# Optimization experiments

Hardware: AMD Instinct MI355X
Metric: run time of the kernel (lower is better)

Reference implementation:

```python
import jax, jax.numpy as jnp
import numpy as np

N_NODES = 100000
N_EDGES = 3200000
B = 64            # number of graphs / RNA batch
DIM = 16          # GINE hidden dim
NFP = 33          # protein node feature dim
EMB = 128         # embedding dim
MAXLEN = 3000     # rna_global length (conv1d in_channels)
LOCLEN = 2998     # rna_local length = 3000 - log4(64) + 1
NF = 32           # n_filters
KS = 8            # conv kernel size -> 128-8+1 = 121
FC_IN = NF * 121  # 3872
BN_EPS = 1e-5


def setup_inputs() -> dict:
    key = jax.random.key(0)
    ks = jax.random.split(key, 32)
    s = 0.1
    p = {}
    # forward data args
    p['pro_x'] = jax.random.normal(ks[0], (N_NODES, NFP), jnp.float32)
    p['pro_edge_index'] = jax.random.randint(ks[1], (2, N_EDGES), 0, N_NODES, jnp.int32)
    p['pro_weight'] = jax.random.uniform(ks[2], (N_EDGES, 1), jnp.float32)
    p['pro_batch'] = jnp.sort(jax.random.randint(ks[3], (N_NODES,), 0, B, jnp.int32))
    p['rna_global'] = jax.random.randint(ks[4], (B, MAXLEN), 0, 5, jnp.int32)
    p['rna_local'] = jax.random.randint(ks[5], (B, LOCLEN), 0, 65, jnp.int32)
    # GINE layer 1 (33 -> 16)
    p['g1_w1'] = jax.random.normal(ks[6], (NFP, DIM), jnp.float32) * s
    p['g1_b1'] = jnp.zeros((DIM,), jnp.float32)
    p['g1_w2'] = jax.random.normal(ks[7], (DIM, DIM), jnp.float32) * s
    p['g1_b2'] = jnp.zeros((DIM,), jnp.float32)
    p['g1_ew'] = jax.random.normal(ks[8], (1, NFP), jnp.float32) * s  # edge Linear(1, 33)
    p['g1_eb'] = jnp.zeros((NFP,), jnp.float32)
    p['g1_eps'] = jnp.zeros((), jnp.float32)
    # GINE layers 2-5 (16 -> 16), stacked on leading axis
    p['g_w1'] = jax.random.normal(ks[9], (4, DIM, DIM), jnp.float32) * s
    p['g_b1'] = jnp.zeros((4, DIM), jnp.float32)
    p['g_w2'] = jax.random.normal(ks[10], (4, DIM, DIM), jnp.float32) * s
    p['g_b2'] = jnp.zeros((4, DIM), jnp.float32)
    p['g_ew'] = jax.random.normal(ks[11], (4, 1, DIM), jnp.float32) * s  # edge Linear(1, 16)
    p['g_eb'] = jnp.zeros((4, DIM), jnp.float32)
    p['g_eps'] = jnp.zeros((4,), jnp.float32)
    # BatchNorm1d x5
    p['bn_gamma'] = jnp.ones((5, DIM), jnp.float32)
    p['bn_beta'] = jnp.zeros((5, DIM), jnp.float32)
    # fc1_xp (16 -> 128)
    p['fc1_xp_w'] = jax.random.normal(ks[12], (DIM, EMB), jnp.float32) * s
    p['fc1_xp_b'] = jnp.zeros((EMB,), jnp.float32)
    # RNA branch
    p['emb1'] = jax.random.normal(ks[13], (5, EMB), jnp.float32)
    p['emb2'] = jax.random.normal(ks[14], (65, EMB), jnp.float32)
    p['convr1_w'] = jax.random.normal(ks[15], (NF, MAXLEN, KS), jnp.float32) * 0.01
    p['convr1_b'] = jnp.zeros((NF,), jnp.float32)
    p['convr2_w'] = jax.random.normal(ks[16], (NF, LOCLEN, KS), jnp.float32) * 0.01
    p['convr2_b'] = jnp.zeros((NF,), jnp.float32)
    p['fcxr_w'] = jax.random.normal(ks[17], (FC_IN, EMB), jnp.float32) * 0.01
    p['fcxr_b'] = jnp.zeros((EMB,), jnp.float32)
    return p


def _gine(x, src, dst, ew, w1, b1, w2, b2, ew_w, ew_b, eps):
    # GINEConv: out = MLP((1+eps)*x + sum_j relu(x_j + edge_lin(e_ij)))
    e = ew @ ew_w + ew_b                       # [E, d]
    m = jax.nn.relu(x[src] + e)                # [E, d] gather + fuse
    agg = jax.ops.segment_sum(m, dst, num_segments=N_NODES)
    h = (1.0 + eps) * x + agg
    return jax.nn.relu(h @ w1 + b1) @ w2 + b2


def _bn(x, gamma, beta):
    mu = jnp.mean(x, axis=0)
    var = jnp.var(x, axis=0)
    return (x - mu) * jax.lax.rsqrt(var + BN_EPS) * gamma + beta


def _rna_branch(tokens, emb, cw, cb, fcw, fcb):
    x = emb[tokens]                            # [B, L, 128]
    y = jax.lax.conv_general_dilated(x, cw, (1,), 'VALID',
                                     dimension_numbers=('NCH', 'OIH', 'NCH'))
    y = y + cb[None, :, None]                  # [B, 32, 121]
    return y.reshape(y.shape[0], -1) @ fcw + fcb


def reference(pro_x, pro_edge_index, pro_weight, pro_batch, rna_global, rna_local,
              g1_w1, g1_b1, g1_w2, g1_b2, g1_ew, g1_eb, g1_eps,
              g_w1, g_b1, g_w2, g_b2, g_ew, g_eb, g_eps,
              bn_gamma, bn_beta, fc1_xp_w, fc1_xp_b,
              emb1, emb2, convr1_w, convr1_b, convr2_w, convr2_b, fcxr_w, fcxr_b):
    src, dst = pro_edge_index[0], pro_edge_index[1]
    # RNA global / local branches (shared fc_xr)
    xrg = _rna_branch(rna_global, emb1, convr1_w, convr1_b, fcxr_w, fcxr_b)
    xrl = _rna_branch(rna_local, emb2, convr2_w, convr2_b, fcxr_w, fcxr_b)
    # protein GINE stack
    xp = jax.nn.relu(_gine(pro_x, src, dst, pro_weight,
                           g1_w1, g1_b1, g1_w2, g1_b2, g1_ew, g1_eb, g1_eps))
    xp = _bn(xp, bn_gamma[0], bn_beta[0])
    for i in range(4):
        xp = jax.nn.relu(_gine(xp, src, dst, pro_weight,
                               g_w1[i], g_b1[i], g_w2[i], g_b2[i],
                               g_ew[i], g_eb[i], g_eps[i]))
        xp = _bn(xp, bn_gamma[i + 1], bn_beta[i + 1])
    # global mean pool over graphs
    sums = jax.ops.segment_sum(xp, pro_batch, num_segments=B)
    cnt = jax.ops.segment_sum(jnp.ones((N_NODES, 1), xp.dtype), pro_batch, num_segments=B)
    xp = jax.nn.relu((sums / jnp.maximum(cnt, 1.0)) @ fc1_xp_w + fc1_xp_b)
    # dropout in eval mode -> identity
    xc_rna = 0.5 * (xrg + xrl)
    return (xc_rna, xp)
```

## Files before the change

### kernel.cpp

```cpp
#include <hip/hip_runtime.h>
#include <hip/hip_fp16.h>

#define N_NODES 100000
#define N_EDGES 3200000
#define BGR 64
#define DIM 16
#define NFP 33
#define ROW1 32
#define H1STR 36
#define EMB 128
#define MAXLEN 3000
#define LOCLEN 2998
#define NF 32
#define KS 8
#define OUTT 121
#define FC_IN 3872
#define BN_EPSV 1e-5f
#define POOL_CHUNK 256
#define POOL_BLKS 391
#define MLPB 391
#define AGGB1 6250
#define AGGB16 3125
#define NBIN 391
#define BCNT_BLK 512
#define P1_CHUNK 4096
#define P1_BLOCKS 782
#define MAXBIN 9088
#define NKC 32
#define KCH 121
#define WDEC (1.f / 32767.f)

__global__ void __launch_bounds__(256) k_bincnt(const int* __restrict__ dst,
                                                int* __restrict__ bh) {
    __shared__ int hist[NBIN];
    int t = threadIdx.x, bid = blockIdx.x;
    for (int b = t; b < NBIN; b += 256) hist[b] = 0;
    __syncthreads();
    int e0 = bid * (N_EDGES / BCNT_BLK);
    int e1 = e0 + (N_EDGES / BCNT_BLK);
    for (int e = e0 + t; e < e1; e += 256) atomicAdd(&hist[dst[e] >> 8], 1);
    __syncthreads();
    for (int b = t; b < NBIN; b += 256) bh[b * BCNT_BLK + bid] = hist[b];
}

__global__ void __launch_bounds__(512) k_binscan(const int* __restrict__ bh,
                                                 int* __restrict__ binoff,
                                                 int* __restrict__ bincur) {
    __shared__ int sc[512];
    int t = threadIdx.x;
    int s = 0;
    if (t < NBIN) {
        const int4* row = (const int4*)(bh + t * BCNT_BLK);
        #pragma unroll 4
        for (int k = 0; k < BCNT_BLK / 4; k++) {
            int4 v = row[k];
            s += v.x + v.y + v.z + v.w;
        }
    }
    sc[t] = s;
    __syncthreads();
    for (int off = 1; off < 512; off <<= 1) {
        int v = (t >= off) ? sc[t - off] : 0;
        __syncthreads();
        sc[t] += v;
        __syncthreads();
    }
    int excl = sc[t] - s;
    if (t <= NBIN) binoff[t] = excl;
    if (t < NBIN) bincur[t] = excl;
}

__global__ void __launch_bounds__(256) k_part1(const int* __restrict__ src,
                                               const int* __restrict__ dst,
                                               const float* __restrict__ w,
                                               int* __restrict__ bincur,
                                               int2* __restrict__ tmp_sw) {
    __shared__ int2 srec[P1_CHUNK];
    __shared__ unsigned short sbin[P1_CHUNK];
    __shared__ unsigned short sperm[P1_CHUNK];
    __shared__ int hist[NBIN];
    __shared__ int off[NBIN];
    __shared__ int cur[NBIN];
    __shared__ int base[NBIN];
    __shared__ int sc[512];
    int t = threadIdx.x;
    int g0 = blockIdx.x * P1_CHUNK;
    int cn = N_EDGES - g0; if (cn > P1_CHUNK) cn = P1_CHUNK;
    for (int b = t; b < NBIN; b += 256) hist[b] = 0;
    __syncthreads();
    for (int j = t; j < cn; j += 256) {
        int d = dst[g0 + j];
        int b = d >> 8;
        sbin[j] = (unsigned short)b;
        srec[j] = make_int2(src[g0 + j] | ((d & 255) << 20), __float_as_int(w[g0 + j]));
        atomicAdd(&hist[b], 1);
    }
    __syncthreads();
    sc[t] = (t < NBIN) ? hist[t] : 0;
    sc[256 + t] = (256 + t < NBIN) ? hist[256 + t] : 0;
    __syncthreads();
    for (int o = 1; o <= 256; o <<= 1) {
        int v0 = (t >= o) ? sc[t - o] : 0;
        int v1 = sc[256 + t - o];
        __syncthreads();
        sc[t] += v0;
        sc[256 + t] += v1;
        __syncthreads();
    }
    for (int b = t; b < NBIN; b += 256) {
        int e = sc[b] - hist[b];
        off[b] = e;
        cur[b] = e;
        int c = hist[b];
        base[b] = c ? atomicAdd(&bincur[b], c) : 0;
    }
    __syncthreads();
    for (int j = t; j < cn; j += 256) {
        int p = atomicAdd(&cur[sbin[j]], 1);
        sperm[p] = (unsigned short)j;
    }
    __syncthreads();
    for (int p = t; p < cn; p += 256) {
        int j = sperm[p];
        int b = sbin[j];
        tmp_sw[base[b] + (p - off[b])] = srec[j];
    }
}

__global__ void __launch_bounds__(256) k_part2(const int2* __restrict__ tmp_sw,
                                               const int* __restrict__ binoff,
                                               unsigned* __restrict__ er,
                                               int* __restrict__ ptr) {
    __shared__ unsigned char sdl[MAXBIN];
    __shared__ unsigned short perm[MAXBIN];
    __shared__ int hist[256];
    __shared__ int cur[256];
    __shared__ int sc[256];
    int t = threadIdx.x, b = blockIdx.x;
    int nlo = b << 8;
    int e0 = binoff[b], e1 = binoff[b + 1];
    int cnt = e1 - e0;
    int stage = cnt < MAXBIN ? cnt : MAXBIN;
    hist[t] = 0;
    __syncthreads();
    for (int j = t; j < stage; j += 256) {
        unsigned char dl = (unsigned char)((tmp_sw[e0 + j].x >> 20) & 255);
        sdl[j] = dl;
        atomicAdd(&hist[dl], 1);
    }
    for (int j = stage + t; j < cnt; j += 256)
        atomicAdd(&hist[(tmp_sw[e0 + j].x >> 20) & 255], 1);
    __syncthreads();
    int v = hist[t];
    sc[t] = v;
    __syncthreads();
    for (int off = 1; off < 256; off <<= 1) {
        int u = (t >= off) ? sc[t - off] : 0;
        __syncthreads();
        sc[t] += u;
        __syncthreads();
    }
    int excl = sc[t] - v;
    cur[t] = excl;
    if (nlo + t < N_NODES) ptr[nlo + t] = e0 + excl;
    if (b == NBIN - 1 && t == 0) ptr[N_NODES] = N_EDGES;
    __syncthreads();
    for (int j = t; j < stage; j += 256) {
        int p = atomicAdd(&cur[sdl[j]], 1);
        perm[p] = (unsigned short)j;
    }
    __syncthreads();
    for (int j = stage + t; j < cnt; j += 256) {
        int2 sw = tmp_sw[e0 + j];
        int p = atomicAdd(&cur[(sw.x >> 20) & 255], 1);
        unsigned wq = (unsigned)(__int_as_float(sw.y) * 32767.f + 0.5f);
        er[e0 + p] = ((unsigned)sw.x & 0x1FFFFu) | (wq << 17);
    }
    for (int p = t; p < stage; p += 256) {
        int2 sw = tmp_sw[e0 + perm[p]];
        unsigned wq = (unsigned)(__int_as_float(sw.y) * 32767.f + 0.5f);
        er[e0 + p] = ((unsigned)sw.x & 0x1FFFFu) | (wq << 17);
    }
}

__global__ void k_half1(const float* __restrict__ x, __half* __restrict__ xh,
                        __half* __restrict__ xh32) {
    int i = blockIdx.x * blockDim.x + threadIdx.x;
    if (i < N_NODES * NFP) {
        int n = i / NFP, f = i - n * NFP;
        __half v = __float2half(x[i]);
        if (f < 32) xh[n * ROW1 + f] = v;
        else xh32[n] = v;
    }
}

__global__ void __launch_bounds__(256) k_cwt(const float* __restrict__ cw,
                                             float* __restrict__ cwT, int L) {
    int l = blockIdx.x;
    int ok = threadIdx.x;
    cwT[l * 256 + ok] = cw[(ok >> 3) * (L * KS) + l * KS + (ok & 7)];
}

__device__ __forceinline__ void acc8p(float a[8], uint4 r, float wv,
                                      const float* __restrict__ ewf,
                                      const float* __restrict__ ebf) {
    float2 f01 = __half22float2(*(__half2*)&r.x);
    float2 f23 = __half22float2(*(__half2*)&r.y);
    float2 f45 = __half22float2(*(__half2*)&r.z);
    float2 f67 = __half22float2(*(__half2*)&r.w);
    float x[8] = {f01.x, f01.y, f23.x, f23.y, f45.x, f45.y, f67.x, f67.y};
    #pragma unroll
    for (int j = 0; j < 8; j++)
        a[j] += fmaxf(x[j] + fmaf(wv, ewf[j], ebf[j]), 0.f);
}

__device__ __forceinline__ void acc8s(float a[8], uint4 r, float wv,
                                      const float* __restrict__ scf,
                                      const float* __restrict__ cbf,
                                      const float* __restrict__ ewf) {
    float2 f01 = __half22float2(*(__half2*)&r.x);
    float2 f23 = __half22float2(*(__half2*)&r.y);
    float2 f45 = __half22float2(*(__half2*)&r.z);
    float2 f67 = __half22float2(*(__half2*)&r.w);
    float x[8] = {f01.x, f01.y, f23.x, f23.y, f45.x, f45.y, f67.x, f67.y};
    #pragma unroll
    for (int j = 0; j < 8; j++)
        a[j] += fmaxf(fmaf(x[j], scf[j], fmaf(wv, ewf[j], cbf[j])), 0.f);
}

__global__ void __launch_bounds__(256) k_agg1(
    const __half* __restrict__ xh, const __half* __restrict__ xh32,
    const int* __restrict__ ptr, const unsigned* __restrict__ er,
    const float* __restrict__ ew, const float* __restrict__ ebv,
    const float* __restrict__ epsp, float* __restrict__ h) {
    int t = threadIdx.x;
    int wave = t >> 6, lane = t & 63;
    int nl = lane >> 4;
    int slot = (lane >> 2) & 3;
    int q = lane & 3;
    float ewf[8], ebf[8];
    #pragma unroll
    for (int j = 0; j < 8; j++) { ewf[j] = ew[q * 8 + j]; ebf[j] = ebv[q * 8 + j]; }
    float ew32 = ew[32], eb32 = ebv[32];
    float ep = 1.f + epsp[0];
    int node = blockIdx.x * 16 + wave * 4 + nl;
    int e0 = ptr[node], e1 = ptr[node + 1];
    float a[8] = {0, 0, 0, 0, 0, 0, 0, 0};
    float a32 = 0.f;
    int i = e0 + slot;
    while (i + 12 < e1) {
        unsigned ev0 = er[i], ev1 = er[i + 4], ev2 = er[i + 8], ev3 = er[i + 12];
        int s0 = ev0 & 0x1FFFF, s1 = ev1 & 0x1FFFF;
        int s2 = ev2 & 0x1FFFF, s3 = ev3 & 0x1FFFF;
        float wv0 = (float)(ev0 >> 17) * WDEC;
        float wv1 = (float)(ev1 >> 17) * WDEC;
        float wv2 = (float)(ev2 >> 17) * WDEC;
        float wv3 = (float)(ev3 >> 17) * WDEC;
        uint4 r0 = *(const uint4*)(xh + s0 * ROW1 + q * 8);
        uint4 r1 = *(const uint4*)(xh + s1 * ROW1 + q * 8);
        uint4 r2 = *(const uint4*)(xh + s2 * ROW1 + q * 8);
        uint4 r3 = *(const uint4*)(xh + s3 * ROW1 + q * 8);
        acc8p(a, r0, wv0, ewf, ebf);
        acc8p(a, r1, wv1, ewf, ebf);
        acc8p(a, r2, wv2, ewf, ebf);
        acc8p(a, r3, wv3, ewf, ebf);
        if (q == 0) {
            a32 += fmaxf(__half2float(xh32[s0]) + fmaf(wv0, ew32, eb32), 0.f);
            a32 += fmaxf(__half2float(xh32[s1]) + fmaf(wv1, ew32, eb32), 0.f);
            a32 += fmaxf(__half2float(xh32[s2]) + fmaf(wv2, ew32, eb32), 0.f);
            a32 += fmaxf(__half2float(xh32[s3]) + fmaf(wv3, ew32, eb32), 0.f);
        }
        i += 16;
    }
    while (i < e1) {
        unsigned ev = er[i];
        int s = ev & 0x1FFFF;
        float wv = (float)(ev >> 17) * WDEC;
        uint4 r = *(const uint4*)(xh + s * ROW1 + q * 8);
        acc8p(a, r, wv, ewf, ebf);
        if (q == 0)
            a32 += fmaxf(__half2float(xh32[s]) + fmaf(wv, ew32, eb32), 0.f);
        i += 4;
    }
    #pragma unroll
    for (int j = 0; j < 8; j++) {
        a[j] += __shfl_xor(a[j], 4);
        a[j] += __shfl_xor(a[j], 8);
    }
    a32 += __shfl_xor(a32, 4);
    a32 += __shfl_xor(a32, 8);
    if (slot == 0) {
        uint4 sraw = *(const uint4*)(xh + node * ROW1 + q * 8);
        float2 s01 = __half22float2(*(__half2*)&sraw.x);
        float2 s23 = __half22float2(*(__half2*)&sraw.y);
        float2 s45 = __half22float2(*(__half2*)&sraw.z);
        float2 s67 = __half22float2(*(__half2*)&sraw.w);
        float* hp = h + node * H1STR + q * 8;
        *(float4*)hp = make_float4(ep * s01.x + a[0], ep * s01.y + a[1],
                                   ep * s23.x + a[2], ep * s23.y + a[3]);
        *(float4*)(hp + 4) = make_float4(ep * s45.x + a[4], ep * s45.y + a[5],
                                         ep * s67.x + a[6], ep * s67.y + a[7]);
        if (q == 0)
            h[node * H1STR + 32] = ep * __half2float(xh32[node]) + a32;
    }
}

__global__ void __launch_bounds__(256) k_agg16(
    const __half* __restrict__ zh, const int* __restrict__ ptr,
    const unsigned* __restrict__ er,
    const float* __restrict__ ew, const float* __restrict__ ebv,
    const float* __restrict__ epsp,
    const float* __restrict__ bnstat, const float* __restrict__ gamma,
    const float* __restrict__ beta, float* __restrict__ h) {
    int t = threadIdx.x;
    int wave = t >> 6, lane = t & 63;
    int nl = lane >> 3;
    int slot = (lane >> 1) & 3;
    int hh = lane & 1;
    float ep = 1.f + epsp[0];
    const float invn = 1.f / (float)N_NODES;
    float scf[8], shf[8], cbf[8], ewf[8];
    #pragma unroll
    for (int j = 0; j < 8; j++) {
        int f = hh * 8 + j;
        float mu = bnstat[f] * invn;
        float var = bnstat[DIM + f] * invn - mu * mu;
        float sc = gamma[f] * rsqrtf(var + BN_EPSV);
        scf[j] = sc;
        shf[j] = beta[f] - mu * sc;
        cbf[j] = shf[j] + ebv[f];
        ewf[j] = ew[f];
    }
    int node = blockIdx.x * 32 + wave * 8 + nl;
    int e0 = ptr[node], e1 = ptr[node + 1];
    float a[8] = {0, 0, 0, 0, 0, 0, 0, 0};
    int i = e0 + slot;
    while (i + 12 < e1) {
        unsigned ev0 = er[i], ev1 = er[i + 4], ev2 = er[i + 8], ev3 = er[i + 12];
        float wv0 = (float)(ev0 >> 17) * WDEC;
        float wv1 = (float)(ev1 >> 17) * WDEC;
        float wv2 = (float)(ev2 >> 17) * WDEC;
        float wv3 = (float)(ev3 >> 17) * WDEC;
        uint4 r0 = *(const uint4*)(zh + (ev0 & 0x1FFFFu) * DIM + hh * 8);
        uint4 r1 = *(const uint4*)(zh + (ev1 & 0x1FFFFu) * DIM + hh * 8);
        uint4 r2 = *(const uint4*)(zh + (ev2 & 0x1FFFFu) * DIM + hh * 8);
        uint4 r3 = *(const uint4*)(zh + (ev3 & 0x1FFFFu) * DIM + hh * 8);
        acc8s(a, r0, wv0, scf, cbf, ewf);
        acc8s(a, r1, wv1, scf, cbf, ewf);
        acc8s(a, r2, wv2, scf, cbf, ewf);
        acc8s(a, r3, wv3, scf, cbf, ewf);
        i += 16;
    }
    while (i < e1) {
        unsigned ev = er[i];
        float wv = (float)(ev >> 17) * WDEC;
        uint4 r = *(const uint4*)(zh + (ev & 0x1FFFFu) * DIM + hh * 8);
        acc8s(a, r, wv, scf, cbf, ewf);
        i += 4;
    }
    #pragma unroll
    for (int j = 0; j < 8; j++) a[j] += __shfl_xor(a[j], 2);
    #pragma unroll
    for (int j = 0; j < 8; j++) a[j] += __shfl_xor(a[j], 4);
    if (slot == 0) {
        uint4 sraw = *(const uint4*)(zh + node * DIM + hh * 8);
        float2 s01 = __half22float2(*(__half2*)&sraw.x);
        float2 s23 = __half22float2(*(__half2*)&sraw.y);
        float2 s45 = __half22float2(*(__half2*)&sraw.z);
        float2 s67 = __half22float2(*(__half2*)&sraw.w);
        float xs[8] = {s01.x, s01.y, s23.x, s23.y, s45.x, s45.y, s67.x, s67.y};
        float o8[8];
        #pragma unroll
        for (int j = 0; j < 8; j++)
            o8[j] = ep * fmaf(xs[j], scf[j], shf[j]) + a[j];
        float* hp = h + node * DIM + hh * 8;
        *(float4*)hp = make_float4(o8[0], o8[1], o8[2], o8[3]);
        *(float4*)(hp + 4) = make_float4(o8[4], o8[5], o8[6], o8[7]);
    }
}

__device__ __forceinline__ void mlp_bn_tail(float zv[16], bool active, int t,
                                            float* __restrict__ part) {
    __shared__ float red[4][32];
    float zs[16], zq[16];
    #pragma unroll
    for (int o = 0; o < 16; o++) {
        zs[o] = active ? zv[o] : 0.f;
        zq[o] = active ? zv[o] * zv[o] : 0.f;
    }
    #pragma unroll
    for (int m = 1; m <= 32; m <<= 1) {
        #pragma unroll
        for (int o = 0; o < 16; o++) {
            zs[o] += __shfl_xor(zs[o], m);
            zq[o] += __shfl_xor(zq[o], m);
        }
    }
    int wave = t >> 6, lane = t & 63;
    if (lane == 0) {
        #pragma unroll
        for (int o = 0; o < 16; o++) {
            red[wave][o] = zs[o];
            red[wave][16 + o] = zq[o];
        }
    }
    __syncthreads();
    if (t < 32)
        part[blockIdx.x * 32 + t] = red[0][t] + red[1][t] + red[2][t] + red[3][t];
}

__device__ __forceinline__ void store_zh(__half* __restrict__ zh, int n, float zv[16]) {
    __half2 p[8];
    #pragma unroll
    for (int j = 0; j < 8; j++) p[j] = __floats2half2_rn(zv[2 * j], zv[2 * j + 1]);
    *(uint4*)(zh + n * DIM) = *(uint4*)&p[0];
    *(uint4*)(zh + n * DIM + 8) = *(uint4*)&p[4];
}

__global__ void __launch_bounds__(256) k_mlp16(
    const float* __restrict__ h,
    const float* __restrict__ W1, const float* __restrict__ b1,
    const float* __restrict__ W2, const float* __restrict__ b2,
    __half* __restrict__ zh, float* __restrict__ part) {
    __shared__ float W1s[256], W2s[256], b1s[16], b2s[16];
    int t = threadIdx.x;
    W1s[t] = W1[t];
    W2s[t] = W2[t];
    if (t < 16) { b1s[t] = b1[t]; b2s[t] = b2[t]; }
    __syncthreads();
    int n = blockIdx.x * 256 + t;
    bool active = n < N_NODES;
    float zv[16];
    if (active) {
        float hv[16];
        #pragma unroll
        for (int j = 0; j < 4; j++) {
            float4 v = *(const float4*)(h + n * DIM + j * 4);
            hv[j * 4] = v.x; hv[j * 4 + 1] = v.y; hv[j * 4 + 2] = v.z; hv[j * 4 + 3] = v.w;
        }
        float tv[16];
        #pragma unroll
        for (int o = 0; o < 16; o++) {
            float s = b1s[o];
            #pragma unroll
            for (int f = 0; f < 16; f++) s += hv[f] * W1s[f * 16 + o];
            tv[o] = fmaxf(s, 0.f);
        }
        #pragma unroll
        for (int o = 0; o < 16; o++) {
            float s = b2s[o];
            #pragma unroll
            for (int f = 0; f < 16; f++) s += tv[f] * W2s[f * 16 + o];
            zv[o] = fmaxf(s, 0.f);
        }
        store_zh(zh, n, zv);
    }
    mlp_bn_tail(zv, active, t, part);
}

__global__ void __launch_bounds__(256) k_mlp1(
    const float* __restrict__ h,
    const float* __restrict__ W1, const float* __restrict__ b1,
    const float* __restrict__ W2, const float* __restrict__ b2,
    __half* __restrict__ zh, float* __restrict__ part) {
    __shared__ float W1s[NFP * 16], W2s[256], b1s[16], b2s[16];
    int t = threadIdx.x;
    for (int j = t; j < NFP * 16; j += 256) W1s[j] = W1[j];
    W2s[t] = W2[t];
    if (t < 16) { b1s[t] = b1[t]; b2s[t] = b2[t]; }
    __syncthreads();
    int n = blockIdx.x * 256 + t;
    bool active = n < N_NODES;
    float zv[16];
    if (active) {
        float hv[NFP];
        #pragma unroll
        for (int j = 0; j < 8; j++) {
            float4 v = *(const float4*)(h + n * H1STR + j * 4);
            hv[j * 4] = v.x; hv[j * 4 + 1] = v.y; hv[j * 4 + 2] = v.z; hv[j * 4 + 3] = v.w;
        }
        hv[32] = h[n * H1STR + 32];
        float tv[16];
        #pragma unroll
        for (int o = 0; o < 16; o++) {
            float s = b1s[o];
            #pragma unroll
            for (int f = 0; f < NFP; f++) s += hv[f] * W1s[f * 16 + o];
            tv[o] = fmaxf(s, 0.f);
        }
        #pragma unroll
        for (int o = 0; o < 16; o++) {
            float s = b2s[o];
            #pragma unroll
            for (int f = 0; f < 16; f++) s += tv[f] * W2s[f * 16 + o];
            zv[o] = fmaxf(s, 0.f);
        }
        store_zh(zh, n, zv);
    }
    mlp_bn_tail(zv, active, t, part);
}

__global__ void __launch_bounds__(1024) k_bnred(const float* __restrict__ part,
                                                float* __restrict__ bnstat) {
    __shared__ float red[1024];
    int t = threadIdx.x;
    int f = t & 31, g = t >> 5;
    float s = 0.f;
    for (int i = g; i < MLPB; i += 32) s += part[i * 32 + f];
    red[t] = s;
    __syncthreads();
    for (int off = 512; off >= 32; off >>= 1) {
        if (t < off) red[t] += red[t + off];
        __syncthreads();
    }
    if (t < 32) bnstat[t] = red[t];
}

__global__ void __launch_bounds__(256) k_pool(const __half* __restrict__ zh,
                                              const int* __restrict__ batch,
                                              const float* __restrict__ bnstat,
                                              const float* __restrict__ gamma,
                                              const float* __restrict__ beta,
                                              float* __restrict__ gsum,
                                              float* __restrict__ gcnt) {
    __shared__ float lsum[BGR * DIM];
    __shared__ float lcnt[BGR];
    int t = threadIdx.x;
    for (int j = t; j < BGR * DIM; j += 256) lsum[j] = 0.f;
    if (t < BGR) lcnt[t] = 0.f;
    __syncthreads();
    int f = t & 15, r = t >> 4;
    const float invn = 1.f / (float)N_NODES;
    float mu = bnstat[f] * invn;
    float var = bnstat[DIM + f] * invn - mu * mu;
    float sc = gamma[f] * rsqrtf(var + BN_EPSV);
    float sh = beta[f] - mu * sc;
    int start = blockIdx.x * POOL_CHUNK;
    float acc = 0.f, cacc = 0.f;
    int cur = -1;
    for (int i = 0; i < POOL_CHUNK / 16; i++) {
        int n = start + r + i * 16;
        if (n >= N_NODES) break;
        int b = batch[n];
        if (b != cur) {
            if (cur >= 0) {
                atomicAdd(&lsum[cur * DIM + f], acc);
                if (f == 0) atomicAdd(&lcnt[cur], cacc);
            }
            cur = b; acc = 0.f; cacc = 0.f;
        }
        acc += fmaf(__half2float(zh[n * DIM + f]), sc, sh);
        cacc += 1.f;
    }
    if (cur >= 0) {
        atomicAdd(&lsum[cur * DIM + f], acc);
        if (f == 0) atomicAdd(&lcnt[cur], cacc);
    }
    __syncthreads();
    for (int j = t; j < BGR * DIM; j += 256) {
        float v = lsum[j];
        if (v != 0.f) atomicAdd(&gsum[j], v);
    }
    if (t < BGR) {
        float v = lcnt[t];
        if (v != 0.f) atomicAdd(&gcnt[t], v);
    }
}

__global__ void k_xp(const float* __restrict__ gsum, const float* __restrict__ gcnt,
                     const float* __restrict__ w, const float* __restrict__ bias,
                     float* __restrict__ out) {
    int b = blockIdx.x;
    int e = threadIdx.x;
    float inv = 1.f / fmaxf(gcnt[b], 1.f);
    float acc = bias[e];
    #pragma unroll
    for (int f = 0; f < DIM; f++) acc += gsum[b * DIM + f] * inv * w[f * EMB + e];
    out[b * EMB + e] = fmaxf(acc, 0.f);
}

__global__ void __launch_bounds__(256) k_bucket(const int* __restrict__ tok, int L, int V,
                                                int* __restrict__ blist,
                                                int* __restrict__ bptr) {
    __shared__ int hist[65];
    __shared__ int cursor[65];
    int b = blockIdx.x, t = threadIdx.x;
    if (t < V) hist[t] = 0;
    __syncthreads();
    for (int l = t; l < L; l += 256) atomicAdd(&hist[tok[b * L + l]], 1);
    __syncthreads();
    if (t == 0) {
        int run = 0;
        for (int v = 0; v < V; v++) {
            cursor[v] = run;
            bptr[b * (V + 1) + v] = run;
            run += hist[v];
        }
        bptr[b * (V + 1) + V] = run;
    }
    __syncthreads();
    for (int l = t; l < L; l += 256) {
        int v = tok[b * L + l];
        int p = atomicAdd(&cursor[v], 1);
        blist[b * L + p] = l;
    }
}

__global__ void __launch_bounds__(256) k_wsum(const int* __restrict__ blist,
                                              const int* __restrict__ bptr,
                                              const float* __restrict__ cwT,
                                              float* __restrict__ W, int L, int V) {
    int b = blockIdx.x, v = blockIdx.y;
    int t = threadIdx.x;
    int s = bptr[b * (V + 1) + v], e = bptr[b * (V + 1) + v + 1];
    const int* bl = blist + b * L;
    float acc = 0.f;
    int j = s;
    while (j + 3 < e) {
        int t0 = bl[j], t1 = bl[j + 1], t2 = bl[j + 2], t3 = bl[j + 3];
        float a0 = cwT[t0 * 256 + t];
        float a1 = cwT[t1 * 256 + t];
        float a2 = cwT[t2 * 256 + t];
        float a3 = cwT[t3 * 256 + t];
        acc += a0 + a1 + a2 + a3;
        j += 4;
    }
    while (j < e) {
        acc += cwT[bl[j] * 256 + t];
        j++;
    }
    int o = t >> 3, k = t & 7;
    W[((b * NF + o) * V + v) * KS + k] = acc;
}

__global__ void k_y(const float* __restrict__ Wg, const float* __restrict__ Wl,
                    const float* __restrict__ emb1, const float* __restrict__ emb2,
                    const float* __restrict__ cb1, const float* __restrict__ cb2,
                    float* __restrict__ yg, float* __restrict__ yl) {
    int which = blockIdx.y;
    int bo = blockIdx.x;
    int b = bo >> 5, o = bo & 31;
    int t = threadIdx.x;
    const float* W = which ? Wl : Wg;
    const float* emb = which ? emb2 : emb1;
    const float* cb = which ? cb2 : cb1;
    float* y = which ? yl : yg;
    int V = which ? 65 : 5;
    __shared__ float Wsh[65 * KS];
    const float* Wrow = W + (b * NF + o) * V * KS;
    for (int j = t; j < V * KS; j += 128) Wsh[j] = Wrow[j];
    __syncthreads();
    if (t < OUTT) {
        float acc = cb[o];
        for (int v = 0; v < V; v++) {
            const float* ep = emb + v * EMB + t;
            #pragma unroll
            for (int k = 0; k < KS; k++) acc += Wsh[v * KS + k] * ep[k];
        }
        y[(b * NF + o) * OUTT + t] = acc;
    }
}

__global__ void __launch_bounds__(128) k_fcpart(const float* __restrict__ yg,
                                                const float* __restrict__ yl,
                                                const float* __restrict__ w,
                                                float* __restrict__ partial) {
    int b = blockIdx.x, which = blockIdx.y, kc = blockIdx.z;
    const float* y = which ? yl : yg;
    int e = threadIdx.x;
    __shared__ float ych[KCH];
    int j0 = kc * KCH;
    if (e < KCH) ych[e] = y[b * FC_IN + j0 + e];
    __syncthreads();
    float acc = 0.f;
    #pragma unroll 4
    for (int jj = 0; jj < KCH; jj++) acc += ych[jj] * w[(j0 + jj) * EMB + e];
    partial[((which * BGR + b) * NKC + kc) * EMB + e] = acc;
}

__global__ void k_fcred(const float* __restrict__ partial, const float* __restrict__ bias,
                        float* __restrict__ out) {
    int b = blockIdx.x;
    int e = threadIdx.x;
    const float* pg = partial + b * NKC * EMB + e;
    const float* pl = partial + (BGR + b) * NKC * EMB + e;
    float ag = bias[e], al = bias[e];
    #pragma unroll
    for (int k = 0; k < NKC; k++) { ag += pg[k * EMB]; al += pl[k * EMB]; }
    out[b * EMB + e] = 0.5f * (ag + al);
}

extern "C" void kernel_launch(void* const* d_in, const int* in_sizes, int n_in,
                              void* d_out, int out_size, void* d_ws, size_t ws_size,
                              hipStream_t stream) {
    const float* pro_x = (const float*)d_in[0];
    const int* eidx = (const int*)d_in[1];
    const int* esrc = eidx;
    const int* edst = eidx + N_EDGES;
    const float* pw = (const float*)d_in[2];
    const int* batch = (const int*)d_in[3];
    const int* rg = (const int*)d_in[4];
    const int* rl = (const int*)d_in[5];
    const float* g1_w1 = (const float*)d_in[6];
    const float* g1_b1 = (const float*)d_in[7];
    const float* g1_w2 = (const float*)d_in[8];
    const float* g1_b2 = (const float*)d_in[9];
    const float* g1_ew = (const float*)d_in[10];
    const float* g1_eb = (const float*)d_in[11];
    const float* g1_eps = (const float*)d_in[12];
    const float* g_w1 = (const float*)d_in[13];
    const float* g_b1 = (const float*)d_in[14];
    const float* g_w2 = (const float*)d_in[15];
    const float* g_b2 = (const float*)d_in[16];
    const float* g_ew = (const float*)d_in[17];
    const float* g_eb = (const float*)d_in[18];
    const float* g_eps = (const float*)d_in[19];
    const float* bn_gamma = (const float*)d_in[20];
    const float* bn_beta = (const float*)d_in[21];
    const float* fc1_xp_w = (const float*)d_in[22];
    const float* fc1_xp_b = (const float*)d_in[23];
    const float* emb1 = (const float*)d_in[24];
    const float* emb2 = (const float*)d_in[25];
    const float* convr1_w = (const float*)d_in[26];
    const float* convr1_b = (const float*)d_in[27];
    const float* convr2_w = (const float*)d_in[28];
    const float* convr2_b = (const float*)d_in[29];
    const float* fcxr_w = (const float*)d_in[30];
    const float* fcxr_b = (const float*)d_in[31];
    float* out = (float*)d_out;

    float* wsf = (float*)d_ws;
    int* ptr       = (int*)wsf;        wsf += 100128;
    int* binoff    = (int*)wsf;        wsf += 512;
    int* bincur    = (int*)wsf;        wsf += 512;
    unsigned* er   = (unsigned*)wsf;   wsf += 2 * N_EDGES;
    float* stats   = wsf;              wsf += 1280;
    float* un = wsf;
    int2* tmp_sw          = (int2*)un;
    int* bh               = (int*)(un + 7200000);
    float* cwTg  = un;
    float* cwTl  = un + 768000;
    __half* zh   = (__half*)(un + 1600000);
    __half* xh1  = (__half*)(un + 2400000);
    __half* xh32 = (__half*)(un + 4000000);
    float* bpart = un + 4100000;
    float* Wg    = un + 4300000;
    float* Wl    = un + 4382000;
    float* yg    = un + 5447000;
    float* yl    = un + 5695000;
    int* blg     = (int*)(un + 5961000);
    int* bll     = (int*)(un + 6153000);
    int* bpg     = (int*)(un + 6345000);
    int* bpl     = (int*)(un + 6346000);
    float* fcpart = un + 6360000;
    float* h      = un + 7400000;
    float* gsum   = stats;
    float* gcnt   = stats + 1024;
    float* bnstat = stats + 1088;

    hipMemsetAsync(stats, 0, 1280 * sizeof(float), stream);

    k_bincnt<<<BCNT_BLK, 256, 0, stream>>>(edst, bh);
    k_binscan<<<1, 512, 0, stream>>>(bh, binoff, bincur);
    k_part1<<<P1_BLOCKS, 256, 0, stream>>>(esrc, edst, pw, bincur, tmp_sw);
    k_part2<<<NBIN, 256, 0, stream>>>(tmp_sw, binoff, er, ptr);

    k_cwt<<<MAXLEN, 256, 0, stream>>>(convr1_w, cwTg, MAXLEN);
    k_cwt<<<LOCLEN, 256, 0, stream>>>(convr2_w, cwTl, LOCLEN);

    k_half1<<<(N_NODES * NFP + 255) / 256, 256, 0, stream>>>(pro_x, xh1, xh32);

    k_bucket<<<BGR, 256, 0, stream>>>(rg, MAXLEN, 5, blg, bpg);
    k_bucket<<<BGR, 256, 0, stream>>>(rl, LOCLEN, 65, bll, bpl);
    k_wsum<<<dim3(BGR, 5), 256, 0, stream>>>(blg, bpg, cwTg, Wg, MAXLEN, 5);
    k_wsum<<<dim3(BGR, 65), 256, 0, stream>>>(bll, bpl, cwTl, Wl, LOCLEN, 65);
    k_y<<<dim3(BGR * NF, 2), 128, 0, stream>>>(Wg, Wl, emb1, emb2, convr1_b, convr2_b, yg, yl);
    k_fcpart<<<dim3(BGR, 2, NKC), 128, 0, stream>>>(yg, yl, fcxr_w, fcpart);
    k_fcred<<<BGR, 128, 0, stream>>>(fcpart, fcxr_b, out);

    k_agg1<<<AGGB1, 256, 0, stream>>>(xh1, xh32, ptr, er, g1_ew, g1_eb, g1_eps, h);
    k_mlp1<<<MLPB, 256, 0, stream>>>(h, g1_w1, g1_b1, g1_w2, g1_b2, zh, bpart);
    k_bnred<<<1, 1024, 0, stream>>>(bpart, bnstat);
    for (int i = 0; i < 4; i++) {
        k_agg16<<<AGGB16, 256, 0, stream>>>(zh, ptr, er,
                                            g_ew + i * DIM, g_eb + i * DIM, g_eps + i,
                                            bnstat + i * 32, bn_gamma + i * DIM,
                                            bn_beta + i * DIM, h);
        k_mlp16<<<MLPB, 256, 0, stream>>>(h, g_w1 + i * DIM * DIM, g_b1 + i * DIM,
                                          g_w2 + i * DIM * DIM, g_b2 + i * DIM, zh, bpart);
        k_bnred<<<1, 1024, 0, stream>>>(bpart, bnstat + (i + 1) * 32);
    }
    k_pool<<<POOL_BLKS, 256, 0, stream>>>(zh, batch, bnstat + 4 * 32,
                                          bn_gamma + 4 * DIM, bn_beta + 4 * DIM, gsum, gcnt);
    k_xp<<<BGR, EMB, 0, stream>>>(gsum, gcnt, fc1_xp_w, fc1_xp_b, out + BGR * EMB);
}
```

Measured before the change: 649.2 us.

## Split global RNA weight-sum into segments and reduce edge-loop unroll to two

The global-RNA k_wsum launch only had 320 blocks, each walking about 600 positions serially. It is now split eight ways per (batch, token), writing partial sums that k_y reduces when it loads its weights. This raises parallelism on the long serial chains. Separately, both GINE aggregation kernels cut their edge-gather unroll from four to two loads per iteration, which lowers register pressure but leaves fewer loads in flight. The workspace layout is reshuffled to fit the larger partial buffer.

```diff
diff --git a/kernel.cpp b/kernel.cpp
--- a/kernel.cpp
+++ b/kernel.cpp
@@ -29,6 +29,7 @@
 #define NKC 32
 #define KCH 121
 #define WDEC (1.f / 32767.f)
+#define SEG_G 8
 
 __global__ void __launch_bounds__(256) k_bincnt(const int* __restrict__ dst,
                                                 int* __restrict__ bh) {
@@ -248,31 +249,23 @@
     float a[8] = {0, 0, 0, 0, 0, 0, 0, 0};
     float a32 = 0.f;
     int i = e0 + slot;
-    while (i + 12 < e1) {
-        unsigned ev0 = er[i], ev1 = er[i + 4], ev2 = er[i + 8], ev3 = er[i + 12];
+    while (i + 4 < e1) {
+        unsigned ev0 = er[i];
+        unsigned ev1 = er[i + 4];
         int s0 = ev0 & 0x1FFFF, s1 = ev1 & 0x1FFFF;
-        int s2 = ev2 & 0x1FFFF, s3 = ev3 & 0x1FFFF;
         float wv0 = (float)(ev0 >> 17) * WDEC;
         float wv1 = (float)(ev1 >> 17) * WDEC;
-        float wv2 = (float)(ev2 >> 17) * WDEC;
-        float wv3 = (float)(ev3 >> 17) * WDEC;
         uint4 r0 = *(const uint4*)(xh + s0 * ROW1 + q * 8);
         uint4 r1 = *(const uint4*)(xh + s1 * ROW1 + q * 8);
-        uint4 r2 = *(const uint4*)(xh + s2 * ROW1 + q * 8);
-        uint4 r3 = *(const uint4*)(xh + s3 * ROW1 + q * 8);
         acc8p(a, r0, wv0, ewf, ebf);
         acc8p(a, r1, wv1, ewf, ebf);
-        acc8p(a, r2, wv2, ewf, ebf);
-        acc8p(a, r3, wv3, ewf, ebf);
         if (q == 0) {
             a32 += fmaxf(__half2float(xh32[s0]) + fmaf(wv0, ew32, eb32), 0.f);
             a32 += fmaxf(__half2float(xh32[s1]) + fmaf(wv1, ew32, eb32), 0.f);
-            a32 += fmaxf(__half2float(xh32[s2]) + fmaf(wv2, ew32, eb32), 0.f);
-            a32 += fmaxf(__half2float(xh32[s3]) + fmaf(wv3, ew32, eb32), 0.f);
-        }
-        i += 16;
-    }
-    while (i < e1) {
+        }
+        i += 8;
+    }
+    if (i < e1) {
         unsigned ev = er[i];
         int s = ev & 0x1FFFF;
         float wv = (float)(ev >> 17) * WDEC;
@@ -280,7 +273,6 @@
         acc8p(a, r, wv, ewf, ebf);
         if (q == 0)
             a32 += fmaxf(__half2float(xh32[s]) + fmaf(wv, ew32, eb32), 0.f);
-        i += 4;
     }
     #pragma unroll
     for (int j = 0; j < 8; j++) {
@@ -335,28 +327,22 @@
     int e0 = ptr[node], e1 = ptr[node + 1];
     float a[8] = {0, 0, 0, 0, 0, 0, 0, 0};
     int i = e0 + slot;
-    while (i + 12 < e1) {
-        unsigned ev0 = er[i], ev1 = er[i + 4], ev2 = er[i + 8], ev3 = er[i + 12];
+    while (i + 4 < e1) {
+        unsigned ev0 = er[i];
+        unsigned ev1 = er[i + 4];
         float wv0 = (float)(ev0 >> 17) * WDEC;
         float wv1 = (float)(ev1 >> 17) * WDEC;
-        float wv2 = (float)(ev2 >> 17) * WDEC;
-        float wv3 = (float)(ev3 >> 17) * WDEC;
         uint4 r0 = *(const uint4*)(zh + (ev0 & 0x1FFFFu) * DIM + hh * 8);
         uint4 r1 = *(const uint4*)(zh + (ev1 & 0x1FFFFu) * DIM + hh * 8);
-        uint4 r2 = *(const uint4*)(zh + (ev2 & 0x1FFFFu) * DIM + hh * 8);
-        uint4 r3 = *(const uint4*)(zh + (ev3 & 0x1FFFFu) * DIM + hh * 8);
         acc8s(a, r0, wv0, scf, cbf, ewf);
         acc8s(a, r1, wv1, scf, cbf, ewf);
-        acc8s(a, r2, wv2, scf, cbf, ewf);
-        acc8s(a, r3, wv3, scf, cbf, ewf);
-        i += 16;
-    }
-    while (i < e1) {
+        i += 8;
+    }
+    if (i < e1) {
         unsigned ev = er[i];
         float wv = (float)(ev >> 17) * WDEC;
         uint4 r = *(const uint4*)(zh + (ev & 0x1FFFFu) * DIM + hh * 8);
         acc8s(a, r, wv, scf, cbf, ewf);
-        i += 4;
     }
     #pragma unroll
     for (int j = 0; j < 8; j++) a[j] += __shfl_xor(a[j], 2);
@@ -606,14 +592,44 @@
     }
 }
 
-__global__ void __launch_bounds__(256) k_wsum(const int* __restrict__ blist,
-                                              const int* __restrict__ bptr,
-                                              const float* __restrict__ cwT,
-                                              float* __restrict__ W, int L, int V) {
+__global__ void __launch_bounds__(256) k_wsum_g(const int* __restrict__ blist,
+                                                const int* __restrict__ bptr,
+                                                const float* __restrict__ cwT,
+                                                float* __restrict__ Wp) {
+    int b = blockIdx.x, v = blockIdx.y, seg = blockIdx.z;
+    int t = threadIdx.x;
+    int s = bptr[b * 6 + v], e = bptr[b * 6 + v + 1];
+    int cnt = e - s;
+    int chunk = (cnt + SEG_G - 1) / SEG_G;
+    int j0 = s + seg * chunk;
+    int j1 = j0 + chunk; if (j1 > e) j1 = e;
+    const int* bl = blist + b * MAXLEN;
+    float acc = 0.f;
+    int j = j0;
+    while (j + 3 < j1) {
+        int t0 = bl[j], t1 = bl[j + 1], t2 = bl[j + 2], t3 = bl[j + 3];
+        float a0 = cwT[t0 * 256 + t];
+        float a1 = cwT[t1 * 256 + t];
+        float a2 = cwT[t2 * 256 + t];
+        float a3 = cwT[t3 * 256 + t];
+        acc += a0 + a1 + a2 + a3;
+        j += 4;
+    }
+    while (j < j1) {
+        acc += cwT[bl[j] * 256 + t];
+        j++;
+    }
+    Wp[((b * 5 + v) * SEG_G + seg) * 256 + t] = acc;
+}
+
+__global__ void __launch_bounds__(256) k_wsum_l(const int* __restrict__ blist,
+                                                const int* __restrict__ bptr,
+                                                const float* __restrict__ cwT,
+                                                float* __restrict__ W) {
     int b = blockIdx.x, v = blockIdx.y;
     int t = threadIdx.x;
-    int s = bptr[b * (V + 1) + v], e = bptr[b * (V + 1) + v + 1];
-    const int* bl = blist + b * L;
+    int s = bptr[b * 66 + v], e = bptr[b * 66 + v + 1];
+    const int* bl = blist + b * LOCLEN;
     float acc = 0.f;
     int j = s;
     while (j + 3 < e) {
@@ -630,10 +646,10 @@
         j++;
     }
     int o = t >> 3, k = t & 7;
-    W[((b * NF + o) * V + v) * KS + k] = acc;
-}
-
-__global__ void k_y(const float* __restrict__ Wg, const float* __restrict__ Wl,
+    W[((b * NF + o) * 65 + v) * KS + k] = acc;
+}
+
+__global__ void k_y(const float* __restrict__ Wpg, const float* __restrict__ Wl,
                     const float* __restrict__ emb1, const float* __restrict__ emb2,
                     const float* __restrict__ cb1, const float* __restrict__ cb2,
                     float* __restrict__ yg, float* __restrict__ yl) {
@@ -641,14 +657,24 @@
     int bo = blockIdx.x;
     int b = bo >> 5, o = bo & 31;
     int t = threadIdx.x;
-    const float* W = which ? Wl : Wg;
     const float* emb = which ? emb2 : emb1;
     const float* cb = which ? cb2 : cb1;
     float* y = which ? yl : yg;
     int V = which ? 65 : 5;
     __shared__ float Wsh[65 * KS];
-    const float* Wrow = W + (b * NF + o) * V * KS;
-    for (int j = t; j < V * KS; j += 128) Wsh[j] = Wrow[j];
+    if (which) {
+        const float* Wrow = Wl + (b * NF + o) * 65 * KS;
+        for (int j = t; j < 65 * KS; j += 128) Wsh[j] = Wrow[j];
+    } else {
+        for (int j = t; j < 5 * KS; j += 128) {
+            int v = j >> 3, k = j & 7;
+            const float* p = Wpg + (b * 5 + v) * SEG_G * 256 + o * 8 + k;
+            float s = 0.f;
+            #pragma unroll
+            for (int g = 0; g < SEG_G; g++) s += p[g * 256];
+            Wsh[j] = s;
+        }
+    }
     __syncthreads();
     if (t < OUTT) {
         float acc = cb[o];
@@ -736,23 +762,23 @@
     unsigned* er   = (unsigned*)wsf;   wsf += 2 * N_EDGES;
     float* stats   = wsf;              wsf += 1280;
     float* un = wsf;
-    int2* tmp_sw          = (int2*)un;
-    int* bh               = (int*)(un + 7200000);
+    int2* tmp_sw = (int2*)un;
+    int* bh      = (int*)(un + 7200000);
     float* cwTg  = un;
     float* cwTl  = un + 768000;
     __half* zh   = (__half*)(un + 1600000);
     __half* xh1  = (__half*)(un + 2400000);
     __half* xh32 = (__half*)(un + 4000000);
     float* bpart = un + 4100000;
-    float* Wg    = un + 4300000;
-    float* Wl    = un + 4382000;
-    float* yg    = un + 5447000;
-    float* yl    = un + 5695000;
-    int* blg     = (int*)(un + 5961000);
-    int* bll     = (int*)(un + 6153000);
-    int* bpg     = (int*)(un + 6345000);
-    int* bpl     = (int*)(un + 6346000);
-    float* fcpart = un + 6360000;
+    float* Wpg   = un + 4300000;
+    float* Wl    = un + 5000000;
+    float* yg    = un + 6100000;
+    float* yl    = un + 6350000;
+    int* blg     = (int*)(un + 6600000);
+    int* bll     = (int*)(un + 6800000);
+    int* bpg     = (int*)(un + 7000000);
+    int* bpl     = (int*)(un + 7001000);
+    float* fcpart = un + 7100000;
     float* h      = un + 7400000;
     float* gsum   = stats;
     float* gcnt   = stats + 1024;
@@ -772,9 +798,9 @@
 
     k_bucket<<<BGR, 256, 0, stream>>>(rg, MAXLEN, 5, blg, bpg);
     k_bucket<<<BGR, 256, 0, stream>>>(rl, LOCLEN, 65, bll, bpl);
-    k_wsum<<<dim3(BGR, 5), 256, 0, stream>>>(blg, bpg, cwTg, Wg, MAXLEN, 5);
-    k_wsum<<<dim3(BGR, 65), 256, 0, stream>>>(bll, bpl, cwTl, Wl, LOCLEN, 65);
-    k_y<<<dim3(BGR * NF, 2), 128, 0, stream>>>(Wg, Wl, emb1, emb2, convr1_b, convr2_b, yg, yl);
+    k_wsum_g<<<dim3(BGR, 5, SEG_G), 256, 0, stream>>>(blg, bpg, cwTg, Wpg);
+    k_wsum_l<<<dim3(BGR, 65), 256, 0, stream>>>(bll, bpl, cwTl, Wl);
+    k_y<<<dim3(BGR * NF, 2), 128, 0, stream>>>(Wpg, Wl, emb1, emb2, convr1_b, convr2_b, yg, yl);
     k_fcpart<<<dim3(BGR, 2, NKC), 128, 0, stream>>>(yg, yl, fcxr_w, fcpart);
     k_fcred<<<BGR, 128, 0, stream>>>(fcpart, fcxr_b, out);
 
```

After: 618.2 us. 1.05x faster.
